# Kernel optimization log

Measured on AMD Instinct MI355X. Metric: run time of the kernel, lower is better.

## Reference

```python
import jax, jax.numpy as jnp
import numpy as np

N = 50000   # nodes
E = 600000  # edges (before self-loops)
D = 128     # input_dim
H = 128     # hidden_dim
NEG_SLOPE = 0.2  # GATConv default


def setup_inputs() -> dict:
    key = jax.random.key(0)
    ks = jax.random.split(key, 16)
    inp = {
        "x": jax.random.normal(ks[0], (N, D), jnp.float32),
        "edge_index": jax.random.randint(ks[1], (2, E), 0, N, dtype=jnp.int64),
        "edge_attr": jax.random.normal(ks[2], (E, 1), jnp.float32),
    }
    # GATConv params per layer: lin W [H,in] (no bias), att_src/att_dst [H],
    # lin_edge We [H,1] (no bias), att_edge [H], final bias b [H]
    def mk(k, shape, fan_in):
        return jax.random.normal(k, shape, jnp.float32) / np.sqrt(fan_in)
    ins = [D, H]
    ki = 3
    for i in range(2):
        cin = ins[i]
        inp[f"W{i}"] = mk(ks[ki], (H, cin), cin); ki += 1
        inp[f"att_src{i}"] = mk(ks[ki], (H,), H); ki += 1
        inp[f"att_dst{i}"] = mk(ks[ki], (H,), H); ki += 1
        inp[f"We{i}"] = mk(ks[ki], (H, 1), 1); ki += 1
        inp[f"att_e{i}"] = mk(ks[ki], (H,), H); ki += 1
        inp[f"b{i}"] = jnp.zeros((H,), jnp.float32)
    return inp


def _gat_forward(x, edge_index, edge_attr, params):
    # add self loops; self-loop edge_attr = mean of edge_attr (fill_value='mean')
    src = jnp.concatenate([edge_index[0], jnp.arange(N, dtype=edge_index.dtype)])
    dst = jnp.concatenate([edge_index[1], jnp.arange(N, dtype=edge_index.dtype)])
    ea = jnp.concatenate(
        [edge_attr, jnp.broadcast_to(edge_attr.mean(0, keepdims=True), (N, 1))], 0
    )  # [E+N, 1]

    def gat_layer(h, W, b, a_s, a_d, We, a_e):
        hp = h @ W.T                                   # [N, H]
        e_lin = ea @ We.T                              # [E+N, H]
        alpha = (hp @ a_s)[src] + (hp @ a_d)[dst] + e_lin @ a_e  # [E+N]
        alpha = jax.nn.leaky_relu(alpha, NEG_SLOPE)
        # segment softmax over destination nodes
        m = jax.ops.segment_max(alpha, dst, num_segments=N)
        m = jnp.where(jnp.isfinite(m), m, 0.0)
        w = jnp.exp(alpha - m[dst])
        denom = jax.ops.segment_sum(w, dst, num_segments=N)
        w = w / (denom[dst] + 1e-16)
        out = jax.ops.segment_sum(hp[src] * w[:, None], dst, num_segments=N)
        return out + b

    layer_outs = [x]
    h = x
    for i in range(2):
        h = jax.nn.relu(
            gat_layer(h, params[f"W{i}"], params[f"b{i}"], params[f"att_src{i}"],
                      params[f"att_dst{i}"], params[f"We{i}"], params[f"att_e{i}"])
        )
        layer_outs.append(h)
    return jnp.concatenate(layer_outs, axis=-1)  # JK 'cat': [N, D + 2H]


def reference(x, edge_index, edge_attr,
              W0, att_src0, att_dst0, We0, att_e0, b0,
              W1, att_src1, att_dst1, We1, att_e1, b1):
    params = {
        "W0": W0, "att_src0": att_src0, "att_dst0": att_dst0, "We0": We0,
        "att_e0": att_e0, "b0": b0,
        "W1": W1, "att_src1": att_src1, "att_dst1": att_dst1, "We1": We1,
        "att_e1": att_e1, "b1": b1,
    }
    return _gat_forward(x, edge_index, edge_attr, params)
```

## Files before the change

### kernel.cpp

```cpp
#include <hip/hip_runtime.h>
#include <hip/hip_fp16.h>
#include <math.h>

#define N_NODES 50000
#define N_EDGES 600000
#define TOT (N_EDGES + N_NODES)
#define HD 128
#define OUTW 384
#define NEG_SLOPE 0.2f


typedef _Float16 h2_t __attribute__((ext_vector_type(2)));

static __device__ __forceinline__ float fdot2f(h2_t a, h2_t b, float c){
#if __has_builtin(__builtin_amdgcn_fdot2)
  return __builtin_amdgcn_fdot2(a, b, c, false);
#else
  return fmaf((float)a[0], (float)b[0], fmaf((float)a[1], (float)b[1], c));
#endif
}

static __device__ __forceinline__ int load_edge(const void* ei, int is64, long long off){
  return is64 ? (int)((const long long*)ei)[off] : ((const int*)ei)[off];
}


__global__ __launch_bounds__(128) void prep_kernel(const void* ei, int* flag,
                                                   const float* __restrict__ We0, const float* __restrict__ ae0,
                                                   const float* __restrict__ We1, const float* __restrict__ ae1,
                                                   float* scal){
  __shared__ float buf[128];
  __shared__ int okbuf;
  int t = threadIdx.x;
  if (t == 0) okbuf = 1;
  __syncthreads();
  if (t < 64){
    long long v = ((const long long*)ei)[t];
    if (v < 0 || v >= N_NODES) atomicAnd(&okbuf, 0);
  }
  buf[t] = We0[t] * ae0[t];
  __syncthreads();
  for (int off = 64; off > 0; off >>= 1){ if (t < off) buf[t] += buf[t + off]; __syncthreads(); }
  if (t == 0) scal[1] = buf[0];
  __syncthreads();
  buf[t] = We1[t] * ae1[t];
  __syncthreads();
  for (int off = 64; off > 0; off >>= 1){ if (t < off) buf[t] += buf[t + off]; __syncthreads(); }
  if (t == 0){ scal[2] = buf[0]; scal[0] = 0.f; *flag = okbuf; }
}

__global__ __launch_bounds__(256) void wconv_kernel(const float* __restrict__ W0, const float* __restrict__ W1,
                                                    __half2* __restrict__ Wt0, __half2* __restrict__ Wt1){
  int e = blockIdx.x * 256 + threadIdx.x;
  if (e >= 16384) return;
  const float* W = (e < 8192) ? W0 : W1;
  __half2* Wt = (e < 8192) ? Wt0 : Wt1;
  int i = e & 8191;
  int n = i & 127, k2 = i >> 7;
  float a = W[n * HD + 2 * k2];
  float b = W[n * HD + 2 * k2 + 1];
  Wt[k2 * 128 + n] = __floats2half2_rn(a, b);
}

__global__ __launch_bounds__(256) void xconv_kernel(const float* __restrict__ x,
                                                    __half* __restrict__ x16,
                                                    float* __restrict__ out){
  int idx = blockIdx.x * 256 + threadIdx.x;
  if (idx >= N_NODES * HD / 4) return;
  int n = idx >> 5, c4 = idx & 31;
  float4 v = ((const float4*)x)[idx];
  *(float4*)&out[(size_t)n * OUTW + c4 * 4] = v;
  float2 pk;
  ((__half2*)&pk)[0] = __floats2half2_rn(v.x, v.y);
  ((__half2*)&pk)[1] = __floats2half2_rn(v.z, v.w);
  *(float2*)&x16[(size_t)idx * 4] = pk;
}

__global__ __launch_bounds__(256) void mean_kernel(const float* __restrict__ ea, float* meansum){
  int tid = blockIdx.x * blockDim.x + threadIdx.x;
  float s = 0.f;
  for (int i = tid; i < N_EDGES; i += gridDim.x * blockDim.x) s += ea[i];
  for (int off = 32; off > 0; off >>= 1) s += __shfl_down(s, off, 64);
  __shared__ float ws[4];
  int lane = threadIdx.x & 63, w = threadIdx.x >> 6;
  if (lane == 0) ws[w] = s;
  __syncthreads();
  if (threadIdx.x == 0){
    atomicAdd(meansum, ws[0] + ws[1] + ws[2] + ws[3]);
  }
}

__global__ __launch_bounds__(256) void degconv_kernel(const void* ei, const int* flag, int* deg,
                                                      int* __restrict__ src32, int* __restrict__ dst32){
  int e = blockIdx.x * 256 + threadIdx.x;
  if (e >= TOT) return;
  int is64 = *flag;
  int d;
  if (e < N_EDGES){
    int s = load_edge(ei, is64, e);
    d = load_edge(ei, is64, (long long)N_EDGES + e);
    src32[e] = s;
    dst32[e] = d;
  } else {
    d = e - N_EDGES;
  }
  atomicAdd(&deg[d], 1);
}

__global__ __launch_bounds__(256) void scan_chunk_kernel(const int* __restrict__ deg,
                                                         int* __restrict__ rowstart,
                                                         int* __restrict__ chunksums){
  __shared__ int sums[256];
  int t = threadIdx.x;
  int base = blockIdx.x * 1024 + t * 4;
  int v[4];
  #pragma unroll
  for (int i = 0; i < 4; i++) v[i] = (base + i < N_NODES) ? deg[base + i] : 0;
  int tsum = v[0] + v[1] + v[2] + v[3];
  sums[t] = tsum;
  __syncthreads();
  for (int off = 1; off < 256; off <<= 1){
    int add = (t >= off) ? sums[t - off] : 0;
    __syncthreads();
    sums[t] += add;
    __syncthreads();
  }
  int run = sums[t] - tsum;
  #pragma unroll
  for (int i = 0; i < 4; i++){
    if (base + i < N_NODES) rowstart[base + i] = run;
    run += v[i];
  }
  if (t == 255) chunksums[blockIdx.x] = sums[255];
}

__global__ void scan_top_kernel(int* chunksums, int nchunks){
  if (threadIdx.x == 0 && blockIdx.x == 0){
    int run = 0;
    for (int c = 0; c < nchunks; c++){ int v = chunksums[c]; chunksums[c] = run; run += v; }
  }
}

__global__ __launch_bounds__(256) void add_off_kernel(int* rowstart, int* rowcur, const int* chunksums){
  int base = blockIdx.x * 1024 + threadIdx.x * 4;
  int off = chunksums[blockIdx.x];
  #pragma unroll
  for (int i = 0; i < 4; i++){
    if (base + i < N_NODES){
      int v = rowstart[base + i] + off;
      rowstart[base + i] = v;
      rowcur[base + i] = v;
    }
  }
}

__global__ __launch_bounds__(256) void fill_kernel(const int* __restrict__ src32,
                                                   const int* __restrict__ dst32,
                                                   int* rowcur, int2* __restrict__ csr){
  int e = blockIdx.x * 256 + threadIdx.x;
  if (e >= TOT) return;
  int s, d;
  if (e < N_EDGES){
    s = src32[e];
    d = dst32[e];
  } else {
    s = d = e - N_EDGES;
  }
  int pos = atomicAdd(&rowcur[d], 1);
  csr[pos] = make_int2(s, e);
}


#define BM 128

__global__ __launch_bounds__(256, 2) void gemm_kernel(const __half* __restrict__ hin,
                                                      const __half2* __restrict__ Wt,
                                                      __half* __restrict__ hp_h,
                                                      const float* __restrict__ as_,
                                                      const float* __restrict__ ad_,
                                                      float* __restrict__ ssrc,
                                                      float* __restrict__ sdst){
  __shared__ __half2 As2[64 * 128];
  __shared__ __half2 Wh2[64 * 128];
  int t  = threadIdx.x;
  int tx = t & 15;
  int ty = t >> 4;
  int rb = blockIdx.x * BM;

  {
    const float4* src = (const float4*)Wt;
    float4* dst = (float4*)Wh2;
    #pragma unroll
    for (int p = 0; p < 8; p++) dst[t + p * 256] = src[t + p * 256];
  }
  #pragma unroll
  for (int p = 0; p < 8; p++){
    int idx = t + p * 256;
    int row = idx >> 4, c8 = idx & 15;
    int gr = rb + row; if (gr >= N_NODES) gr = N_NODES - 1;
    float4 v = *(const float4*)&hin[(size_t)gr * HD + c8 * 8];
    __half2* hv = (__half2*)&v;
    #pragma unroll
    for (int q = 0; q < 4; q++) As2[(4 * c8 + q) * 128 + row] = hv[q];
  }
  __syncthreads();

  float acc[8][8];
  #pragma unroll
  for (int i = 0; i < 8; i++)
    #pragma unroll
    for (int j = 0; j < 8; j++) acc[i][j] = 0.f;

  #pragma unroll 4
  for (int k2 = 0; k2 < 64; k2++){
    float4 ar0 = *(const float4*)&As2[k2 * 128 + ty * 8];
    float4 ar1 = *(const float4*)&As2[k2 * 128 + ty * 8 + 4];
    float4 wr0 = *(const float4*)&Wh2[k2 * 128 + tx * 4];
    float4 wr1 = *(const float4*)&Wh2[k2 * 128 + 64 + tx * 4];
    const h2_t* av0 = (const h2_t*)&ar0;
    const h2_t* av1 = (const h2_t*)&ar1;
    const h2_t* wv0 = (const h2_t*)&wr0;
    const h2_t* wv1 = (const h2_t*)&wr1;
    #pragma unroll
    for (int i = 0; i < 8; i++){
      h2_t ai = (i < 4) ? av0[i] : av1[i - 4];
      #pragma unroll
      for (int j = 0; j < 4; j++){
        acc[i][j]     = fdot2f(ai, wv0[j], acc[i][j]);
        acc[i][j + 4] = fdot2f(ai, wv1[j], acc[i][j + 4]);
      }
    }
  }

  #pragma unroll
  for (int i = 0; i < 8; i++){
    int r = rb + ty * 8 + i;
    if (r < N_NODES){
      float2 s0, s1;
      ((__half2*)&s0)[0] = __floats2half2_rn(acc[i][0], acc[i][1]);
      ((__half2*)&s0)[1] = __floats2half2_rn(acc[i][2], acc[i][3]);
      ((__half2*)&s1)[0] = __floats2half2_rn(acc[i][4], acc[i][5]);
      ((__half2*)&s1)[1] = __floats2half2_rn(acc[i][6], acc[i][7]);
      *(float2*)&hp_h[(size_t)r * HD + tx * 4]      = s0;
      *(float2*)&hp_h[(size_t)r * HD + 64 + tx * 4] = s1;
    }
  }

  float as_v[8], ad_v[8];
  #pragma unroll
  for (int j = 0; j < 4; j++){
    as_v[j]     = as_[tx * 4 + j];      ad_v[j]     = ad_[tx * 4 + j];
    as_v[j + 4] = as_[64 + tx * 4 + j]; ad_v[j + 4] = ad_[64 + tx * 4 + j];
  }
  #pragma unroll
  for (int i = 0; i < 8; i++){
    float ps = 0.f, pd = 0.f;
    #pragma unroll
    for (int j = 0; j < 8; j++){
      ps = fmaf(acc[i][j], as_v[j], ps);
      pd = fmaf(acc[i][j], ad_v[j], pd);
    }
    #pragma unroll
    for (int off = 8; off > 0; off >>= 1){
      ps += __shfl_down(ps, off, 16);
      pd += __shfl_down(pd, off, 16);
    }
    int r = rb + ty * 8 + i;
    if (tx == 0 && r < N_NODES){ ssrc[r] = ps; sdst[r] = pd; }
  }
}

__global__ __launch_bounds__(256) void attn_kernel(const int* __restrict__ rowstart,
                                                   const int2* __restrict__ csr,
                                                   const float* __restrict__ eattr,
                                                   const float* __restrict__ ssrc,
                                                   const float* __restrict__ sdst,
                                                   const float* __restrict__ scal, int which,
                                                   float* __restrict__ wp,
                                                   float* __restrict__ pinv){
  int sub  = threadIdx.x >> 4;
  int lane = threadIdx.x & 15;
  int n = blockIdx.x * 16 + sub;
  if (n >= N_NODES) return;
  int s0 = rowstart[n];
  int s1 = (n + 1 < N_NODES) ? rowstart[n + 1] : TOT;
  float sd = sdst[n];
  float ce = scal[1 + which];
  float mean_ea = scal[0] * (1.0f / (float)N_EDGES);
  float sum = 0.f;
  for (int i = s0 + lane; i < s1; i += 16){
    int2 se = csr[i];
    float eav = (se.y < N_EDGES) ? eattr[se.y] : mean_ea;
    float a = ssrc[se.x] + sd + eav * ce;
    a = (a >= 0.f) ? a : NEG_SLOPE * a;
    float w = expf(a);
    wp[i] = w;
    sum += w;
  }
  #pragma unroll
  for (int off = 8; off > 0; off >>= 1) sum += __shfl_xor(sum, off, 16);
  if (lane == 0) pinv[n] = 1.0f / (sum + 1e-16f);
}

__global__ __launch_bounds__(256) void agg_kernel(const int* __restrict__ rowstart,
                                                  const int2* __restrict__ csr,
                                                  const float* __restrict__ wp,
                                                  const float* __restrict__ pinv,
                                                  const __half* __restrict__ hp_h,
                                                  const float* __restrict__ bias,
                                                  __half* __restrict__ hnext,
                                                  float* __restrict__ out, int outoff){
  int sub  = threadIdx.x >> 4;
  int lane = threadIdx.x & 15;
  int n = blockIdx.x * 16 + sub;
  if (n >= N_NODES) return;
  int s0 = rowstart[n];
  int s1 = (n + 1 < N_NODES) ? rowstart[n + 1] : TOT;
  const float4* hb = (const float4*)hp_h;

  float a0 = 0.f, a1 = 0.f, a2 = 0.f, a3 = 0.f;
  float a4 = 0.f, a5 = 0.f, a6 = 0.f, a7 = 0.f;

#define ACC8(r, p) { const __half2* hh = (const __half2*)&(r); float2 f;         \
    f = __half22float2(hh[0]); a0 = fmaf(p, f.x, a0); a1 = fmaf(p, f.y, a1);     \
    f = __half22float2(hh[1]); a2 = fmaf(p, f.x, a2); a3 = fmaf(p, f.y, a3);     \
    f = __half22float2(hh[2]); a4 = fmaf(p, f.x, a4); a5 = fmaf(p, f.y, a5);     \
    f = __half22float2(hh[3]); a6 = fmaf(p, f.x, a6); a7 = fmaf(p, f.y, a7); }

  int i = s0;
  for (; i + 4 <= s1; i += 4){
    int2 se0 = csr[i],     se1 = csr[i + 1];
    int2 se2 = csr[i + 2], se3 = csr[i + 3];
    float p0 = wp[i],     p1 = wp[i + 1];
    float p2 = wp[i + 2], p3 = wp[i + 3];
    float4 r0 = hb[(size_t)se0.x * 16 + lane];
    float4 r1 = hb[(size_t)se1.x * 16 + lane];
    float4 r2 = hb[(size_t)se2.x * 16 + lane];
    float4 r3 = hb[(size_t)se3.x * 16 + lane];
    ACC8(r0, p0); ACC8(r1, p1); ACC8(r2, p2); ACC8(r3, p3);
  }
  for (; i < s1; i++){
    int2 se = csr[i];
    float p = wp[i];
    float4 r = hb[(size_t)se.x * 16 + lane];
    ACC8(r, p);
  }
#undef ACC8

  float inv = pinv[n];
  float4 bA = *(const float4*)&bias[lane * 8];
  float4 bB = *(const float4*)&bias[lane * 8 + 4];
  float v0 = fmaf(a0, inv, bA.x); v0 = v0 > 0.f ? v0 : 0.f;
  float v1 = fmaf(a1, inv, bA.y); v1 = v1 > 0.f ? v1 : 0.f;
  float v2 = fmaf(a2, inv, bA.z); v2 = v2 > 0.f ? v2 : 0.f;
  float v3 = fmaf(a3, inv, bA.w); v3 = v3 > 0.f ? v3 : 0.f;
  float v4 = fmaf(a4, inv, bB.x); v4 = v4 > 0.f ? v4 : 0.f;
  float v5 = fmaf(a5, inv, bB.y); v5 = v5 > 0.f ? v5 : 0.f;
  float v6 = fmaf(a6, inv, bB.z); v6 = v6 > 0.f ? v6 : 0.f;
  float v7 = fmaf(a7, inv, bB.w); v7 = v7 > 0.f ? v7 : 0.f;
  if (hnext){
    float4 pk;
    __half2* p2h = (__half2*)&pk;
    p2h[0] = __floats2half2_rn(v0, v1);
    p2h[1] = __floats2half2_rn(v2, v3);
    p2h[2] = __floats2half2_rn(v4, v5);
    p2h[3] = __floats2half2_rn(v6, v7);
    *(float4*)&hnext[(size_t)n * HD + lane * 8] = pk;
  }
  *(float4*)&out[(size_t)n * OUTW + outoff + lane * 8]     = make_float4(v0, v1, v2, v3);
  *(float4*)&out[(size_t)n * OUTW + outoff + lane * 8 + 4] = make_float4(v4, v5, v6, v7);
}


extern "C" void kernel_launch(void* const* d_in, const int* in_sizes, int n_in,
                              void* d_out, int out_size, void* d_ws, size_t ws_size,
                              hipStream_t stream){
  (void)in_sizes; (void)n_in; (void)out_size; (void)ws_size;
  const float* x    = (const float*)d_in[0];
  const void*  ei   = d_in[1];
  const float* eatt = (const float*)d_in[2];
  const float* W0   = (const float*)d_in[3];
  const float* as0  = (const float*)d_in[4];
  const float* ad0  = (const float*)d_in[5];
  const float* We0  = (const float*)d_in[6];
  const float* ae0  = (const float*)d_in[7];
  const float* b0   = (const float*)d_in[8];
  const float* W1   = (const float*)d_in[9];
  const float* as1  = (const float*)d_in[10];
  const float* ad1  = (const float*)d_in[11];
  const float* We1  = (const float*)d_in[12];
  const float* ae1  = (const float*)d_in[13];
  const float* b1   = (const float*)d_in[14];
  float* out = (float*)d_out;

  char* ws = (char*)d_ws;
  size_t off = 0;
  auto alloc = [&](size_t bytes) -> void* {
    void* p = ws + off;
    off += (bytes + 255) & ~(size_t)255;
    return p;
  };
  __half*   hp_h     = (__half*)  alloc((size_t)N_NODES * HD * 2);
  __half*   h1       = (__half*)  alloc((size_t)N_NODES * HD * 2);
  __half*   x16      = (__half*)  alloc((size_t)N_NODES * HD * 2);
  float*    ssrc     = (float*)   alloc((size_t)N_NODES * 4);
  float*    sdst     = (float*)   alloc((size_t)N_NODES * 4);
  float*    wp       = (float*)   alloc((size_t)TOT * 4);
  float*    pinv     = (float*)   alloc((size_t)N_NODES * 4);
  int*      deg      = (int*)     alloc((size_t)N_NODES * 4);
  int*      rowstart = (int*)     alloc((size_t)N_NODES * 4);
  int*      rowcur   = (int*)     alloc((size_t)N_NODES * 4);
  int*      src32    = (int*)     alloc((size_t)N_EDGES * 4);
  int*      dst32    = (int*)     alloc((size_t)N_EDGES * 4);
  int2*     csr      = (int2*)    alloc((size_t)TOT * 8);
  __half2*  Wt0      = (__half2*) alloc((size_t)8192 * 4);
  __half2*  Wt1      = (__half2*) alloc((size_t)8192 * 4);
  int*      chunksums= (int*)     alloc(64 * 4);
  float*    scal     = (float*)   alloc(64 * 4);
  int*      flag     = (int*)     alloc(64);

  hipMemsetAsync(deg, 0, (size_t)N_NODES * 4, stream);

  const int EB = (TOT + 255) / 256;
  const int nchunks = (N_NODES + 1023) / 1024;

  prep_kernel<<<1, 128, 0, stream>>>(ei, flag, We0, ae0, We1, ae1, scal);
  wconv_kernel<<<64, 256, 0, stream>>>(W0, W1, Wt0, Wt1);
  xconv_kernel<<<(N_NODES * HD / 4 + 255) / 256, 256, 0, stream>>>(x, x16, out);
  mean_kernel<<<256, 256, 0, stream>>>(eatt, scal);
  degconv_kernel<<<EB, 256, 0, stream>>>(ei, flag, deg, src32, dst32);
  scan_chunk_kernel<<<nchunks, 256, 0, stream>>>(deg, rowstart, chunksums);
  scan_top_kernel<<<1, 64, 0, stream>>>(chunksums, nchunks);
  add_off_kernel<<<nchunks, 256, 0, stream>>>(rowstart, rowcur, chunksums);
  fill_kernel<<<EB, 256, 0, stream>>>(src32, dst32, rowcur, csr);

  const int GB = (N_NODES + BM - 1) / BM;
  const int NB16 = (N_NODES + 15) / 16;

  gemm_kernel<<<GB, 256, 0, stream>>>(x16, Wt0, hp_h, as0, ad0, ssrc, sdst);
  attn_kernel<<<NB16, 256, 0, stream>>>(rowstart, csr, eatt, ssrc, sdst, scal, 0, wp, pinv);
  agg_kernel<<<NB16, 256, 0, stream>>>(rowstart, csr, wp, pinv, hp_h, b0, h1, out, 128);

  gemm_kernel<<<GB, 256, 0, stream>>>(h1, Wt1, hp_h, as1, ad1, ssrc, sdst);
  attn_kernel<<<NB16, 256, 0, stream>>>(rowstart, csr, eatt, ssrc, sdst, scal, 1, wp, pinv);
  agg_kernel<<<NB16, 256, 0, stream>>>(rowstart, csr, wp, pinv, hp_h, b1, nullptr, out, 256);
}
```

Before: 340.6 us.

## Fuse attention weights into aggregation and merge setup kernels to cut launches

Removes attn_kernel and instead recomputes each edge weight (leaky-relu plus exp) and its softmax denominator inside agg_kernel, so the wp and pinv intermediate buffers are no longer written and read back. The setup kernels are merged: the mean reduction moves into prep_kernel, and x/W conversion and degree counting are combined into one conv_kernel dispatched by block index. scan_top is dropped; add_off now sums the chunk prefixes itself with a warp reduction. A single memset now zeroes both deg and the adjacent scal. The trade-off is that each of the 16 lanes per node recomputes the exp and the ssrc/eattr gathers for every edge, and the code depends on deg and scal staying contiguous in the workspace.

```diff
diff --git a/kernel.cpp b/kernel.cpp
--- a/kernel.cpp
+++ b/kernel.cpp
@@ -25,86 +25,85 @@
 }
 
 
-__global__ __launch_bounds__(128) void prep_kernel(const void* ei, int* flag,
+__global__ __launch_bounds__(256) void prep_kernel(const void* ei, int* flag,
                                                    const float* __restrict__ We0, const float* __restrict__ ae0,
                                                    const float* __restrict__ We1, const float* __restrict__ ae1,
-                                                   float* scal){
-  __shared__ float buf[128];
-  __shared__ int okbuf;
+                                                   float* scal, const float* __restrict__ eattr){
   int t = threadIdx.x;
-  if (t == 0) okbuf = 1;
-  __syncthreads();
-  if (t < 64){
-    long long v = ((const long long*)ei)[t];
-    if (v < 0 || v >= N_NODES) atomicAnd(&okbuf, 0);
-  }
-  buf[t] = We0[t] * ae0[t];
-  __syncthreads();
-  for (int off = 64; off > 0; off >>= 1){ if (t < off) buf[t] += buf[t + off]; __syncthreads(); }
-  if (t == 0) scal[1] = buf[0];
-  __syncthreads();
-  buf[t] = We1[t] * ae1[t];
-  __syncthreads();
-  for (int off = 64; off > 0; off >>= 1){ if (t < off) buf[t] += buf[t + off]; __syncthreads(); }
-  if (t == 0){ scal[2] = buf[0]; scal[0] = 0.f; *flag = okbuf; }
-}
-
-__global__ __launch_bounds__(256) void wconv_kernel(const float* __restrict__ W0, const float* __restrict__ W1,
-                                                    __half2* __restrict__ Wt0, __half2* __restrict__ Wt1){
-  int e = blockIdx.x * 256 + threadIdx.x;
-  if (e >= 16384) return;
-  const float* W = (e < 8192) ? W0 : W1;
-  __half2* Wt = (e < 8192) ? Wt0 : Wt1;
-  int i = e & 8191;
-  int n = i & 127, k2 = i >> 7;
-  float a = W[n * HD + 2 * k2];
-  float b = W[n * HD + 2 * k2 + 1];
-  Wt[k2 * 128 + n] = __floats2half2_rn(a, b);
-}
-
-__global__ __launch_bounds__(256) void xconv_kernel(const float* __restrict__ x,
-                                                    __half* __restrict__ x16,
-                                                    float* __restrict__ out){
-  int idx = blockIdx.x * 256 + threadIdx.x;
-  if (idx >= N_NODES * HD / 4) return;
-  int n = idx >> 5, c4 = idx & 31;
-  float4 v = ((const float4*)x)[idx];
-  *(float4*)&out[(size_t)n * OUTW + c4 * 4] = v;
-  float2 pk;
-  ((__half2*)&pk)[0] = __floats2half2_rn(v.x, v.y);
-  ((__half2*)&pk)[1] = __floats2half2_rn(v.z, v.w);
-  *(float2*)&x16[(size_t)idx * 4] = pk;
-}
-
-__global__ __launch_bounds__(256) void mean_kernel(const float* __restrict__ ea, float* meansum){
-  int tid = blockIdx.x * blockDim.x + threadIdx.x;
+  if (blockIdx.x == 0){
+    __shared__ float buf[128];
+    __shared__ int okbuf;
+    if (t == 0) okbuf = 1;
+    __syncthreads();
+    if (t < 64){
+      long long v = ((const long long*)ei)[t];
+      if (v < 0 || v >= N_NODES) atomicAnd(&okbuf, 0);
+    }
+    if (t < 128) buf[t] = We0[t] * ae0[t];
+    __syncthreads();
+    for (int off = 64; off > 0; off >>= 1){ if (t < off) buf[t] += buf[t + off]; __syncthreads(); }
+    if (t == 0) scal[1] = buf[0];
+    __syncthreads();
+    if (t < 128) buf[t] = We1[t] * ae1[t];
+    __syncthreads();
+    for (int off = 64; off > 0; off >>= 1){ if (t < off) buf[t] += buf[t + off]; __syncthreads(); }
+    if (t == 0){ scal[2] = buf[0]; *flag = okbuf; }
+  }
+  int tid = blockIdx.x * 256 + t;
   float s = 0.f;
-  for (int i = tid; i < N_EDGES; i += gridDim.x * blockDim.x) s += ea[i];
+  for (int i = tid; i < N_EDGES; i += 256 * 256) s += eattr[i];
   for (int off = 32; off > 0; off >>= 1) s += __shfl_down(s, off, 64);
   __shared__ float ws[4];
-  int lane = threadIdx.x & 63, w = threadIdx.x >> 6;
+  int lane = t & 63, w = t >> 6;
   if (lane == 0) ws[w] = s;
   __syncthreads();
-  if (threadIdx.x == 0){
-    atomicAdd(meansum, ws[0] + ws[1] + ws[2] + ws[3]);
-  }
-}
-
-__global__ __launch_bounds__(256) void degconv_kernel(const void* ei, const int* flag, int* deg,
-                                                      int* __restrict__ src32, int* __restrict__ dst32){
-  int e = blockIdx.x * 256 + threadIdx.x;
-  if (e >= TOT) return;
-  int is64 = *flag;
-  int d;
-  if (e < N_EDGES){
-    int s = load_edge(ei, is64, e);
-    d = load_edge(ei, is64, (long long)N_EDGES + e);
-    src32[e] = s;
-    dst32[e] = d;
+  if (t == 0) atomicAdd(&scal[0], ws[0] + ws[1] + ws[2] + ws[3]);
+}
+
+#define XBLK 6250
+#define WBLK 64
+#define DBLK 2540
+__global__ __launch_bounds__(256) void conv_kernel(const float* __restrict__ x,
+                                                   __half* __restrict__ x16,
+                                                   float* __restrict__ out,
+                                                   const float* __restrict__ W0, const float* __restrict__ W1,
+                                                   __half2* __restrict__ Wt0, __half2* __restrict__ Wt1,
+                                                   const void* ei, const int* flag, int* deg,
+                                                   int* __restrict__ src32, int* __restrict__ dst32){
+  int b = blockIdx.x;
+  if (b < XBLK){
+    int idx = b * 256 + threadIdx.x;
+    int n = idx >> 5, c4 = idx & 31;
+    float4 v = ((const float4*)x)[idx];
+    *(float4*)&out[(size_t)n * OUTW + c4 * 4] = v;
+    float2 pk;
+    ((__half2*)&pk)[0] = __floats2half2_rn(v.x, v.y);
+    ((__half2*)&pk)[1] = __floats2half2_rn(v.z, v.w);
+    *(float2*)&x16[(size_t)idx * 4] = pk;
+  } else if (b < XBLK + WBLK){
+    int e = (b - XBLK) * 256 + threadIdx.x;
+    const float* W = (e < 8192) ? W0 : W1;
+    __half2* Wt = (e < 8192) ? Wt0 : Wt1;
+    int i = e & 8191;
+    int n = i & 127, k2 = i >> 7;
+    float a = W[n * HD + 2 * k2];
+    float c = W[n * HD + 2 * k2 + 1];
+    Wt[k2 * 128 + n] = __floats2half2_rn(a, c);
   } else {
-    d = e - N_EDGES;
-  }
-  atomicAdd(&deg[d], 1);
+    int e = (b - XBLK - WBLK) * 256 + threadIdx.x;
+    if (e >= TOT) return;
+    int is64 = *flag;
+    int d;
+    if (e < N_EDGES){
+      int s = load_edge(ei, is64, e);
+      d = load_edge(ei, is64, (long long)N_EDGES + e);
+      src32[e] = s;
+      dst32[e] = d;
+    } else {
+      d = e - N_EDGES;
+    }
+    atomicAdd(&deg[d], 1);
+  }
 }
 
 __global__ __launch_bounds__(256) void scan_chunk_kernel(const int* __restrict__ deg,
@@ -134,16 +133,18 @@
   if (t == 255) chunksums[blockIdx.x] = sums[255];
 }
 
-__global__ void scan_top_kernel(int* chunksums, int nchunks){
-  if (threadIdx.x == 0 && blockIdx.x == 0){
-    int run = 0;
-    for (int c = 0; c < nchunks; c++){ int v = chunksums[c]; chunksums[c] = run; run += v; }
-  }
-}
-
-__global__ __launch_bounds__(256) void add_off_kernel(int* rowstart, int* rowcur, const int* chunksums){
-  int base = blockIdx.x * 1024 + threadIdx.x * 4;
-  int off = chunksums[blockIdx.x];
+__global__ __launch_bounds__(256) void add_off_kernel(int* rowstart, int* rowcur,
+                                                      const int* __restrict__ chunksums){
+  __shared__ int soff;
+  int t = threadIdx.x;
+  if (t < 64){
+    int v = (t < blockIdx.x) ? chunksums[t] : 0;
+    for (int o = 32; o > 0; o >>= 1) v += __shfl_down(v, o, 64);
+    if (t == 0) soff = v;
+  }
+  __syncthreads();
+  int off = soff;
+  int base = blockIdx.x * 1024 + t * 4;
   #pragma unroll
   for (int i = 0; i < 4; i++){
     if (base + i < N_NODES){
@@ -270,42 +271,12 @@
   }
 }
 
-__global__ __launch_bounds__(256) void attn_kernel(const int* __restrict__ rowstart,
-                                                   const int2* __restrict__ csr,
-                                                   const float* __restrict__ eattr,
-                                                   const float* __restrict__ ssrc,
-                                                   const float* __restrict__ sdst,
-                                                   const float* __restrict__ scal, int which,
-                                                   float* __restrict__ wp,
-                                                   float* __restrict__ pinv){
-  int sub  = threadIdx.x >> 4;
-  int lane = threadIdx.x & 15;
-  int n = blockIdx.x * 16 + sub;
-  if (n >= N_NODES) return;
-  int s0 = rowstart[n];
-  int s1 = (n + 1 < N_NODES) ? rowstart[n + 1] : TOT;
-  float sd = sdst[n];
-  float ce = scal[1 + which];
-  float mean_ea = scal[0] * (1.0f / (float)N_EDGES);
-  float sum = 0.f;
-  for (int i = s0 + lane; i < s1; i += 16){
-    int2 se = csr[i];
-    float eav = (se.y < N_EDGES) ? eattr[se.y] : mean_ea;
-    float a = ssrc[se.x] + sd + eav * ce;
-    a = (a >= 0.f) ? a : NEG_SLOPE * a;
-    float w = expf(a);
-    wp[i] = w;
-    sum += w;
-  }
-  #pragma unroll
-  for (int off = 8; off > 0; off >>= 1) sum += __shfl_xor(sum, off, 16);
-  if (lane == 0) pinv[n] = 1.0f / (sum + 1e-16f);
-}
-
 __global__ __launch_bounds__(256) void agg_kernel(const int* __restrict__ rowstart,
                                                   const int2* __restrict__ csr,
-                                                  const float* __restrict__ wp,
-                                                  const float* __restrict__ pinv,
+                                                  const float* __restrict__ eattr,
+                                                  const float* __restrict__ ssrc,
+                                                  const float* __restrict__ sdst,
+                                                  const float* __restrict__ scal, int which,
                                                   const __half* __restrict__ hp_h,
                                                   const float* __restrict__ bias,
                                                   __half* __restrict__ hnext,
@@ -316,10 +287,19 @@
   if (n >= N_NODES) return;
   int s0 = rowstart[n];
   int s1 = (n + 1 < N_NODES) ? rowstart[n + 1] : TOT;
+  float sd = sdst[n];
+  float ce = scal[1 + which];
+  float mean_ea = scal[0] * (1.0f / (float)N_EDGES);
   const float4* hb = (const float4*)hp_h;
 
   float a0 = 0.f, a1 = 0.f, a2 = 0.f, a3 = 0.f;
   float a4 = 0.f, a5 = 0.f, a6 = 0.f, a7 = 0.f;
+  float sum = 0.f;
+
+#define EW(se) ({ float eav = ((se).y < N_EDGES) ? eattr[(se).y] : mean_ea;       \
+    float al = ssrc[(se).x] + sd + eav * ce;                                      \
+    al = (al >= 0.f) ? al : NEG_SLOPE * al;                                       \
+    expf(al); })
 
 #define ACC8(r, p) { const __half2* hh = (const __half2*)&(r); float2 f;         \
     f = __half22float2(hh[0]); a0 = fmaf(p, f.x, a0); a1 = fmaf(p, f.y, a1);     \
@@ -331,23 +311,25 @@
   for (; i + 4 <= s1; i += 4){
     int2 se0 = csr[i],     se1 = csr[i + 1];
     int2 se2 = csr[i + 2], se3 = csr[i + 3];
-    float p0 = wp[i],     p1 = wp[i + 1];
-    float p2 = wp[i + 2], p3 = wp[i + 3];
     float4 r0 = hb[(size_t)se0.x * 16 + lane];
     float4 r1 = hb[(size_t)se1.x * 16 + lane];
     float4 r2 = hb[(size_t)se2.x * 16 + lane];
     float4 r3 = hb[(size_t)se3.x * 16 + lane];
+    float p0 = EW(se0), p1 = EW(se1), p2 = EW(se2), p3 = EW(se3);
+    sum += p0 + p1 + p2 + p3;
     ACC8(r0, p0); ACC8(r1, p1); ACC8(r2, p2); ACC8(r3, p3);
   }
   for (; i < s1; i++){
     int2 se = csr[i];
-    float p = wp[i];
     float4 r = hb[(size_t)se.x * 16 + lane];
+    float p = EW(se);
+    sum += p;
     ACC8(r, p);
   }
 #undef ACC8
-
-  float inv = pinv[n];
+#undef EW
+
+  float inv = 1.0f / (sum + 1e-16f);
   float4 bA = *(const float4*)&bias[lane * 8];
   float4 bB = *(const float4*)&bias[lane * 8 + 4];
   float v0 = fmaf(a0, inv, bA.x); v0 = v0 > 0.f ? v0 : 0.f;
@@ -405,9 +387,8 @@
   __half*   x16      = (__half*)  alloc((size_t)N_NODES * HD * 2);
   float*    ssrc     = (float*)   alloc((size_t)N_NODES * 4);
   float*    sdst     = (float*)   alloc((size_t)N_NODES * 4);
-  float*    wp       = (float*)   alloc((size_t)TOT * 4);
-  float*    pinv     = (float*)   alloc((size_t)N_NODES * 4);
   int*      deg      = (int*)     alloc((size_t)N_NODES * 4);
+  float*    scal     = (float*)   alloc(64 * 4);
   int*      rowstart = (int*)     alloc((size_t)N_NODES * 4);
   int*      rowcur   = (int*)     alloc((size_t)N_NODES * 4);
   int*      src32    = (int*)     alloc((size_t)N_EDGES * 4);
@@ -416,32 +397,26 @@
   __half2*  Wt0      = (__half2*) alloc((size_t)8192 * 4);
   __half2*  Wt1      = (__half2*) alloc((size_t)8192 * 4);
   int*      chunksums= (int*)     alloc(64 * 4);
-  float*    scal     = (float*)   alloc(64 * 4);
   int*      flag     = (int*)     alloc(64);
 
-  hipMemsetAsync(deg, 0, (size_t)N_NODES * 4, stream);
-
-  const int EB = (TOT + 255) / 256;
+  hipMemsetAsync(deg, 0, 200192 + 256, stream);
+
   const int nchunks = (N_NODES + 1023) / 1024;
-
-  prep_kernel<<<1, 128, 0, stream>>>(ei, flag, We0, ae0, We1, ae1, scal);
-  wconv_kernel<<<64, 256, 0, stream>>>(W0, W1, Wt0, Wt1);
-  xconv_kernel<<<(N_NODES * HD / 4 + 255) / 256, 256, 0, stream>>>(x, x16, out);
-  mean_kernel<<<256, 256, 0, stream>>>(eatt, scal);
-  degconv_kernel<<<EB, 256, 0, stream>>>(ei, flag, deg, src32, dst32);
+  const int FB = (TOT + 255) / 256;
+
+  prep_kernel<<<256, 256, 0, stream>>>(ei, flag, We0, ae0, We1, ae1, scal, eatt);
+  conv_kernel<<<XBLK + WBLK + DBLK, 256, 0, stream>>>(x, x16, out, W0, W1, Wt0, Wt1,
+                                                      ei, flag, deg, src32, dst32);
   scan_chunk_kernel<<<nchunks, 256, 0, stream>>>(deg, rowstart, chunksums);
-  scan_top_kernel<<<1, 64, 0, stream>>>(chunksums, nchunks);
   add_off_kernel<<<nchunks, 256, 0, stream>>>(rowstart, rowcur, chunksums);
-  fill_kernel<<<EB, 256, 0, stream>>>(src32, dst32, rowcur, csr);
+  fill_kernel<<<FB, 256, 0, stream>>>(src32, dst32, rowcur, csr);
 
   const int GB = (N_NODES + BM - 1) / BM;
   const int NB16 = (N_NODES + 15) / 16;
 
   gemm_kernel<<<GB, 256, 0, stream>>>(x16, Wt0, hp_h, as0, ad0, ssrc, sdst);
-  attn_kernel<<<NB16, 256, 0, stream>>>(rowstart, csr, eatt, ssrc, sdst, scal, 0, wp, pinv);
-  agg_kernel<<<NB16, 256, 0, stream>>>(rowstart, csr, wp, pinv, hp_h, b0, h1, out, 128);
+  agg_kernel<<<NB16, 256, 0, stream>>>(rowstart, csr, eatt, ssrc, sdst, scal, 0, hp_h, b0, h1, out, 128);
 
   gemm_kernel<<<GB, 256, 0, stream>>>(h1, Wt1, hp_h, as1, ad1, ssrc, sdst);
-  attn_kernel<<<NB16, 256, 0, stream>>>(rowstart, csr, eatt, ssrc, sdst, scal, 1, wp, pinv);
-  agg_kernel<<<NB16, 256, 0, stream>>>(rowstart, csr, wp, pinv, hp_h, b1, nullptr, out, 256);
-}
+  agg_kernel<<<NB16, 256, 0, stream>>>(rowstart, csr, eatt, ssrc, sdst, scal, 1, hp_h, b1, nullptr, out, 256);
+}
```

New measurement: 324.6 us. 1.05x faster.
